# Performance work log

Measured on AMD Instinct MI355X. Metric: run time of the kernel, lower is better.

Reference implementation:

```python
import jax, jax.numpy as jnp
import numpy as np

NEG_SLOPE = 0.2  # PyG GATConv LeakyReLU slope
BN_EPS = 1e-5
NUM_GRAPHS = 16


def gat_conv(x, src, dst, W, a_src, a_dst, bias, heads, out_c, concat):
    N = x.shape[0]
    h = (x @ W).reshape(N, heads, out_c)                      # [N,H,C]
    s_src = jnp.sum(h * a_src, axis=-1)                       # [N,H] per-node src score
    s_dst = jnp.sum(h * a_dst, axis=-1)                       # [N,H]
    e = jax.nn.leaky_relu(s_src[src] + s_dst[dst], NEG_SLOPE) # [E,H]
    # segment softmax over incoming edges of each dst node
    m = jax.ops.segment_max(e, dst, num_segments=N)           # [N,H]
    ex = jnp.exp(e - m[dst])
    denom = jax.ops.segment_sum(ex, dst, num_segments=N)      # [N,H]
    alpha = ex / (denom[dst] + 1e-16)                         # [E,H]
    msg = h[src] * alpha[:, :, None]                          # [E,H,C]
    out = jax.ops.segment_sum(msg, dst, num_segments=N)       # [N,H,C]
    out = out.reshape(N, heads * out_c) if concat else out.mean(axis=1)
    return out + bias


def batchnorm_eval(x, gamma, beta, rm, rv):
    return (x - rm) * jax.lax.rsqrt(rv + BN_EPS) * gamma + beta


def setup_inputs() -> dict:
    key = jax.random.key(0)
    ks = jax.random.split(key, 16)
    N, E, Fin, Hc, Hd, Emb = 20000, 640000, 128, 64, 4, 128
    x = jax.random.normal(ks[0], (N, Fin), dtype=jnp.float32)
    edge_index = jax.random.randint(ks[1], (2, E), 0, N, dtype=jnp.int64)
    batch = jnp.sort(jax.random.randint(ks[2], (N,), 0, NUM_GRAPHS, dtype=jnp.int64))
    sc1 = 1.0 / np.sqrt(Fin)
    sc2 = 1.0 / np.sqrt(Hc * Hd)
    return {
        "x": x, "edge_index": edge_index, "batch": batch,
        "W1": jax.random.normal(ks[3], (Fin, Hd * Hc), dtype=jnp.float32) * sc1,
        "a_src1": jax.random.normal(ks[4], (Hd, Hc), dtype=jnp.float32) * sc2,
        "a_dst1": jax.random.normal(ks[5], (Hd, Hc), dtype=jnp.float32) * sc2,
        "b1": jnp.zeros((Hd * Hc,), jnp.float32),
        "g1": jnp.ones((Hd * Hc,), jnp.float32),
        "be1": jnp.zeros((Hd * Hc,), jnp.float32),
        "rm1": jax.random.normal(ks[6], (Hd * Hc,), dtype=jnp.float32) * 0.1,
        "rv1": jnp.ones((Hd * Hc,), jnp.float32),
        "W2": jax.random.normal(ks[7], (Hd * Hc, Emb), dtype=jnp.float32) * sc2,
        "a_src2": jax.random.normal(ks[8], (1, Emb), dtype=jnp.float32) / np.sqrt(Emb),
        "a_dst2": jax.random.normal(ks[9], (1, Emb), dtype=jnp.float32) / np.sqrt(Emb),
        "b2": jnp.zeros((Emb,), jnp.float32),
        "g2": jnp.ones((Emb,), jnp.float32),
        "be2": jnp.zeros((Emb,), jnp.float32),
        "rm2": jax.random.normal(ks[10], (Emb,), dtype=jnp.float32) * 0.1,
        "rv2": jnp.ones((Emb,), jnp.float32),
    }


def reference(x, edge_index, batch, W1, a_src1, a_dst1, b1, g1, be1, rm1, rv1,
              W2, a_src2, a_dst2, b2, g2, be2, rm2, rv2):
    N = x.shape[0]
    loops = jnp.arange(N, dtype=edge_index.dtype)
    src = jnp.concatenate([edge_index[0], loops])  # PyG GATConv adds self-loops
    dst = jnp.concatenate([edge_index[1], loops])
    # layer 1: heads=4, concat
    h = gat_conv(x, src, dst, W1, a_src1, a_dst1, b1, heads=4, out_c=64, concat=True)
    h = batchnorm_eval(h, g1, be1, rm1, rv1)
    h = jax.nn.elu(h)  # dropout is identity in eval mode
    # layer 2: heads=1, no concat (mean over heads)
    h = gat_conv(h, src, dst, W2, a_src2, a_dst2, b2, heads=1, out_c=128, concat=False)
    h = batchnorm_eval(h, g2, be2, rm2, rv2)
    # global mean pool per graph
    sums = jax.ops.segment_sum(h, batch, num_segments=NUM_GRAPHS)
    cnts = jax.ops.segment_sum(jnp.ones((N,), h.dtype), batch, num_segments=NUM_GRAPHS)
    return sums / jnp.maximum(cnts, 1.0)[:, None]
```

## Files before the change

kernel.cpp:

```cpp
#include <hip/hip_runtime.h>
#include <hip/hip_bf16.h>
#include <math.h>

#define NEG_SLOPE 0.2f
#define BN_EPS 1e-5f
#define ELLW 128
#define SCLAMP 60.0f
#define LDP 68

typedef __attribute__((ext_vector_type(8))) short bf16x8;
typedef __attribute__((ext_vector_type(4))) float f32x4;

__device__ __forceinline__ void atomAddF(float* p, float v) { unsafeAtomicAdd(p, v); }
__device__ __forceinline__ float bf_lo(unsigned u) { return __uint_as_float(u << 16); }
__device__ __forceinline__ float bf_hi(unsigned u) { return __uint_as_float(u & 0xffff0000u); }
__device__ __forceinline__ float lk(float x) { return x > 0.f ? x : NEG_SLOPE * x; }
__device__ __forceinline__ float eexp(float x) { return __expf(fminf(x, SCLAMP)); }

__global__ __launch_bounds__(256) void prep_kernel(const float* __restrict__ x,
                                                   const float* __restrict__ W1,
                                                   const float* __restrict__ W2,
                                                   const int* __restrict__ src,
                                                   const int* __restrict__ dst,
                                                   __hip_bfloat16* __restrict__ xbf,
                                                   __hip_bfloat16* __restrict__ WT1,
                                                   __hip_bfloat16* __restrict__ WT2,
                                                   int* __restrict__ cnt,
                                                   int* __restrict__ ell,
                                                   int n4, int E, int Etot) {
    int i = blockIdx.x * blockDim.x + threadIdx.x;
    if (i < n4) {
        float4 v = ((const float4*)x)[i];
        ushort4 st;
        st.x = __bfloat16_as_ushort(__float2bfloat16(v.x));
        st.y = __bfloat16_as_ushort(__float2bfloat16(v.y));
        st.z = __bfloat16_as_ushort(__float2bfloat16(v.z));
        st.w = __bfloat16_as_ushort(__float2bfloat16(v.w));
        *(ushort4*)(xbf + (size_t)i * 4) = st;
        return;
    }
    int j = i - n4;
    if (j < 128 * 256) {
        int k = j >> 8, n = j & 255;
        WT1[(size_t)n * 128 + k] = __float2bfloat16(W1[j]);
        return;
    }
    j -= 128 * 256;
    if (j < 256 * 128) {
        int k = j >> 7, n = j & 127;
        WT2[(size_t)n * 256 + k] = __float2bfloat16(W2[j]);
        return;
    }
    j -= 256 * 128;
    if (j < Etot) {
        int s, d;
        if (j < E) { s = src[j]; d = dst[j]; } else { s = d = j - E; }
        int pos = atomicAdd(cnt + d, 1);
        if (pos < ELLW) ell[(size_t)d * ELLW + pos] = s;
    }
}

__global__ __launch_bounds__(256) void gemm_score_kernel(const __hip_bfloat16* __restrict__ A,
                                                         const __hip_bfloat16* __restrict__ BT,
                                                         __hip_bfloat16* __restrict__ C,
                                                         const float* __restrict__ asrc,
                                                         const float* __restrict__ adst,
                                                         float* __restrict__ ssrc,
                                                         float* __restrict__ sdst,
                                                         int M, int N, int K, int heads) {
    __shared__ __hip_bfloat16 As[64 * LDP];
    __shared__ __hip_bfloat16 Bs[64 * LDP];
    const int tid = threadIdx.x;
    const int w = tid >> 6;
    const int lane = tid & 63;
    const int q = lane >> 4;
    const int r16 = lane & 15;
    const int bm = blockIdx.y * 64;
    const int bn = blockIdx.x * 64;
    const int lrow = tid >> 3;
    const int lseg = tid & 7;
    f32x4 acc[4] = {};

    for (int k0 = 0; k0 < K; k0 += 64) {
#pragma unroll
        for (int half = 0; half < 2; ++half) {
            int row = lrow + half * 32;
            int ga = min(bm + row, M - 1);
            *(bf16x8*)(&As[row * LDP + lseg * 8]) =
                *(const bf16x8*)(A + (size_t)ga * K + k0 + lseg * 8);
            *(bf16x8*)(&Bs[row * LDP + lseg * 8]) =
                *(const bf16x8*)(BT + (size_t)(bn + row) * K + k0 + lseg * 8);
        }
        __syncthreads();
#pragma unroll
        for (int kk = 0; kk < 64; kk += 32) {
            bf16x8 a = *(const bf16x8*)(&As[(w * 16 + r16) * LDP + kk + q * 8]);
#pragma unroll
            for (int t = 0; t < 4; ++t) {
                bf16x8 b = *(const bf16x8*)(&Bs[(t * 16 + r16) * LDP + kk + q * 8]);
                acc[t] = __builtin_amdgcn_mfma_f32_16x16x32_bf16(a, b, acc[t], 0, 0, 0);
            }
        }
        __syncthreads();
    }
#pragma unroll
    for (int t = 0; t < 4; ++t)
#pragma unroll
        for (int r = 0; r < 4; ++r) {
            int row = bm + w * 16 + q * 4 + r;
            if (row < M)
                C[(size_t)row * N + bn + t * 16 + r16] = __float2bfloat16(acc[t][r]);
        }
    if (heads) {
        const int h = (heads == 4) ? blockIdx.x : 0;
        float asv[4], adv[4];
#pragma unroll
        for (int t = 0; t < 4; ++t) {
            int col = bn + t * 16 + r16;
            asv[t] = asrc[col]; adv[t] = adst[col];
        }
#pragma unroll
        for (int r = 0; r < 4; ++r) {
            int row = bm + w * 16 + q * 4 + r;
            float ss = 0.f, sd = 0.f;
#pragma unroll
            for (int t = 0; t < 4; ++t) { ss += acc[t][r] * asv[t]; sd += acc[t][r] * adv[t]; }
#pragma unroll
            for (int mask = 1; mask <= 8; mask <<= 1) {
                ss += __shfl_xor(ss, mask);
                sd += __shfl_xor(sd, mask);
            }
            if (r16 == 0 && row < M) {
                atomAddF(&ssrc[(size_t)row * heads + h], ss);
                atomAddF(&sdst[(size_t)row * heads + h], sd);
            }
        }
    }
}

__global__ __launch_bounds__(256) void fused1_kernel(const int* __restrict__ ell,
                                                     const int* __restrict__ cnt,
                                                     const float* __restrict__ ssrc,
                                                     const float* __restrict__ sdst,
                                                     const __hip_bfloat16* __restrict__ h1,
                                                     const float* __restrict__ b,
                                                     const float* __restrict__ g,
                                                     const float* __restrict__ be,
                                                     const float* __restrict__ rm,
                                                     const float* __restrict__ rv,
                                                     __hip_bfloat16* __restrict__ out1,
                                                     int N) {
    __shared__ float4 sex[4][ELLW];
    const int w = threadIdx.x >> 6;
    const int lane = threadIdx.x & 63;
    const int n = blockIdx.x * 4 + w;
    if (n >= N) return;
    const int degn = min(cnt[n], ELLW);
    const int* __restrict__ row = ell + (size_t)n * ELLW;
    const float4 sd4 = *(const float4*)(sdst + (size_t)n * 4);

    float4 d4 = {0.f, 0.f, 0.f, 0.f};
    for (int i = lane; i < degn; i += 64) {
        int s = row[i];
        float4 sc = *(const float4*)(ssrc + (size_t)s * 4);
        float4 e4;
        e4.x = eexp(lk(sc.x + sd4.x)); e4.y = eexp(lk(sc.y + sd4.y));
        e4.z = eexp(lk(sc.z + sd4.z)); e4.w = eexp(lk(sc.w + sd4.w));
        sex[w][i] = e4;
        d4.x += e4.x; d4.y += e4.y; d4.z += e4.z; d4.w += e4.w;
    }
#pragma unroll
    for (int o = 32; o; o >>= 1) {
        d4.x += __shfl_xor(d4.x, o); d4.y += __shfl_xor(d4.y, o);
        d4.z += __shfl_xor(d4.z, o); d4.w += __shfl_xor(d4.w, o);
    }

    const int h = lane >> 4, c16 = lane & 15;
    const int ch = h * 64 + c16 * 4;
    const float denh = h == 0 ? d4.x : h == 1 ? d4.y : h == 2 ? d4.z : d4.w;
    const float rden = 1.f / (denh + 1e-16f);
    const __hip_bfloat16* hbase = h1 + ch;
    const float* exw = (const float*)&sex[w][0];

    f32x4 acc = {0.f, 0.f, 0.f, 0.f};
    int i = 0;
    for (; i + 7 < degn; i += 8) {
        int s[8]; float a[8]; uint2 u[8];
#pragma unroll
        for (int k = 0; k < 8; ++k) { s[k] = row[i + k]; a[k] = exw[(i + k) * 4 + h]; }
#pragma unroll
        for (int k = 0; k < 8; ++k) u[k] = *(const uint2*)(hbase + (size_t)s[k] * 256);
#pragma unroll
        for (int k = 0; k < 8; ++k) {
            acc.x += a[k] * bf_lo(u[k].x); acc.y += a[k] * bf_hi(u[k].x);
            acc.z += a[k] * bf_lo(u[k].y); acc.w += a[k] * bf_hi(u[k].y);
        }
    }
    for (; i < degn; ++i) {
        int s0 = row[i];
        float a0 = exw[i * 4 + h];
        uint2 u0 = *(const uint2*)(hbase + (size_t)s0 * 256);
        acc.x += a0 * bf_lo(u0.x); acc.y += a0 * bf_hi(u0.x);
        acc.z += a0 * bf_lo(u0.y); acc.w += a0 * bf_hi(u0.y);
    }
    float4 bb = *(const float4*)(b + ch), gg = *(const float4*)(g + ch);
    float4 ee = *(const float4*)(be + ch), mm = *(const float4*)(rm + ch);
    float4 vv = *(const float4*)(rv + ch);
    float o0 = (acc.x * rden + bb.x - mm.x) * rsqrtf(vv.x + BN_EPS) * gg.x + ee.x;
    float o1 = (acc.y * rden + bb.y - mm.y) * rsqrtf(vv.y + BN_EPS) * gg.y + ee.y;
    float o2 = (acc.z * rden + bb.z - mm.z) * rsqrtf(vv.z + BN_EPS) * gg.z + ee.z;
    float o3 = (acc.w * rden + bb.w - mm.w) * rsqrtf(vv.w + BN_EPS) * gg.w + ee.w;
    o0 = o0 > 0.f ? o0 : expm1f(o0);
    o1 = o1 > 0.f ? o1 : expm1f(o1);
    o2 = o2 > 0.f ? o2 : expm1f(o2);
    o3 = o3 > 0.f ? o3 : expm1f(o3);
    ushort4 st;
    st.x = __bfloat16_as_ushort(__float2bfloat16(o0));
    st.y = __bfloat16_as_ushort(__float2bfloat16(o1));
    st.z = __bfloat16_as_ushort(__float2bfloat16(o2));
    st.w = __bfloat16_as_ushort(__float2bfloat16(o3));
    *(ushort4*)(out1 + (size_t)n * 256 + ch) = st;
}

__global__ __launch_bounds__(256) void fused2_kernel(const int* __restrict__ ell,
                                                     const int* __restrict__ cnt,
                                                     const float* __restrict__ ssrc,
                                                     const float* __restrict__ sdst,
                                                     const __hip_bfloat16* __restrict__ h2,
                                                     const float* __restrict__ b,
                                                     const float* __restrict__ g,
                                                     const float* __restrict__ be,
                                                     const float* __restrict__ rm,
                                                     const float* __restrict__ rv,
                                                     float* __restrict__ out2,
                                                     int N) {
    __shared__ float sex[4][ELLW];
    const int w = threadIdx.x >> 6;
    const int lane = threadIdx.x & 63;
    const int n = blockIdx.x * 4 + w;
    if (n >= N) return;
    const int degn = min(cnt[n], ELLW);
    const int* __restrict__ row = ell + (size_t)n * ELLW;
    const float sd = sdst[n];

    float den = 0.f;
    for (int i = lane; i < degn; i += 64) {
        int s = row[i];
        float e = eexp(lk(ssrc[s] + sd));
        sex[w][i] = e;
        den += e;
    }
#pragma unroll
    for (int o = 32; o; o >>= 1) den += __shfl_xor(den, o);
    const float rden = 1.f / (den + 1e-16f);

    const int ch = lane * 2;
    const __hip_bfloat16* hbase = h2 + ch;
    float ax = 0.f, ay = 0.f;
    int i = 0;
    for (; i + 7 < degn; i += 8) {
        int s[8]; float a[8]; unsigned u[8];
#pragma unroll
        for (int k = 0; k < 8; ++k) { s[k] = row[i + k]; a[k] = sex[w][i + k]; }
#pragma unroll
        for (int k = 0; k < 8; ++k) u[k] = *(const unsigned*)(hbase + (size_t)s[k] * 128);
#pragma unroll
        for (int k = 0; k < 8; ++k) { ax += a[k] * bf_lo(u[k]); ay += a[k] * bf_hi(u[k]); }
    }
    for (; i < degn; ++i) {
        int s0 = row[i];
        float a0 = sex[w][i];
        unsigned u0 = *(const unsigned*)(hbase + (size_t)s0 * 128);
        ax += a0 * bf_lo(u0); ay += a0 * bf_hi(u0);
    }
    float2 bb = *(const float2*)(b + ch), gg = *(const float2*)(g + ch);
    float2 ee = *(const float2*)(be + ch), mm = *(const float2*)(rm + ch);
    float2 vv = *(const float2*)(rv + ch);
    float2 o;
    o.x = (ax * rden + bb.x - mm.x) * rsqrtf(vv.x + BN_EPS) * gg.x + ee.x;
    o.y = (ay * rden + bb.y - mm.y) * rsqrtf(vv.y + BN_EPS) * gg.y + ee.y;
    *(float2*)(out2 + (size_t)n * 128 + ch) = o;
}

__global__ __launch_bounds__(128) void pool_kernel(const float* __restrict__ out2,
                                                   const int* __restrict__ batch,
                                                   float* __restrict__ pool,
                                                   int N, int npb) {
    const int j = threadIdx.x;
    int n0 = blockIdx.x * npb;
    int n1 = min(n0 + npb, N);
    if (n0 >= n1) return;
    int curg = batch[n0];
    float acc = 0.f;
    for (int n = n0; n < n1; ++n) {
        int gr = batch[n];
        if (gr != curg) {
            atomAddF(pool + (size_t)curg * 128 + j, acc);
            acc = 0.f; curg = gr;
        }
        acc += out2[(size_t)n * 128 + j];
    }
    atomAddF(pool + (size_t)curg * 128 + j, acc);
}

__device__ __forceinline__ int lowerBound(const int* __restrict__ a, int n, int v) {
    int lo = 0, hi = n;
    while (lo < hi) {
        int mid = (lo + hi) >> 1;
        if (a[mid] < v) lo = mid + 1; else hi = mid;
    }
    return lo;
}

__global__ __launch_bounds__(256) void final_kernel(const float* __restrict__ pool,
                                                    const int* __restrict__ batch,
                                                    float* __restrict__ out, int N) {
    int i = blockIdx.x * blockDim.x + threadIdx.x;
    int g = i >> 7;
    int c = lowerBound(batch, N, g + 1) - lowerBound(batch, N, g);
    out[i] = pool[i] / fmaxf((float)c, 1.f);
}

extern "C" void kernel_launch(void* const* d_in, const int* in_sizes, int n_in,
                              void* d_out, int out_size, void* d_ws, size_t ws_size,
                              hipStream_t stream) {
    const float* x    = (const float*)d_in[0];
    const int* ei     = (const int*)d_in[1];
    const int* batch  = (const int*)d_in[2];
    const float* W1   = (const float*)d_in[3];
    const float* as1  = (const float*)d_in[4];
    const float* ad1  = (const float*)d_in[5];
    const float* b1   = (const float*)d_in[6];
    const float* g1   = (const float*)d_in[7];
    const float* be1  = (const float*)d_in[8];
    const float* rm1  = (const float*)d_in[9];
    const float* rv1  = (const float*)d_in[10];
    const float* W2   = (const float*)d_in[11];
    const float* as2  = (const float*)d_in[12];
    const float* ad2  = (const float*)d_in[13];
    const float* b2   = (const float*)d_in[14];
    const float* g2   = (const float*)d_in[15];
    const float* be2  = (const float*)d_in[16];
    const float* rm2  = (const float*)d_in[17];
    const float* rv2  = (const float*)d_in[18];
    float* out = (float*)d_out;

    const int N = in_sizes[0] / 128;
    const int E = in_sizes[1] / 2;
    const int Etot = E + N;
    const int* src = ei;
    const int* dst = ei + E;

    char* p = (char*)d_ws;
    auto alloc = [&](size_t bytes) { char* r = p; p += (bytes + 255) & ~(size_t)255; return r; };
    __hip_bfloat16* h1   = (__hip_bfloat16*)alloc((size_t)N * 256 * 2);
    __hip_bfloat16* out1 = (__hip_bfloat16*)alloc((size_t)N * 256 * 2);
    float* out2          = (float*)alloc((size_t)N * 128 * 4);
    __hip_bfloat16* xbf  = (__hip_bfloat16*)alloc((size_t)N * 128 * 2);
    __hip_bfloat16* WT1  = (__hip_bfloat16*)alloc(256 * 128 * 2);
    __hip_bfloat16* WT2  = (__hip_bfloat16*)alloc(128 * 256 * 2);
    char* zbase          = alloc((size_t)N * 10 * 4 + 2048 * 4 + (size_t)N * 4);
    float* ssrc1         = (float*)zbase;
    float* sdst1         = ssrc1 + (size_t)N * 4;
    float* ssrc2         = sdst1 + (size_t)N * 4;
    float* sdst2         = ssrc2 + N;
    float* pool          = sdst2 + N;
    int*   cnt           = (int*)(pool + 2048);
    int*   ell           = (int*)alloc((size_t)N * ELLW * 4);
    __hip_bfloat16* h2   = h1;

    const size_t zbytes = (size_t)N * 10 * 4 + 2048 * 4 + (size_t)N * 4;
    hipMemsetAsync(zbase, 0, zbytes, stream);

    const int n4 = N * 128 / 4;
    const int ptot = n4 + 2 * 128 * 256 + Etot;
    prep_kernel<<<(ptot + 255) / 256, 256, 0, stream>>>(x, W1, W2, src, dst, xbf, WT1, WT2,
                                                        cnt, ell, n4, E, Etot);

    gemm_score_kernel<<<dim3(256 / 64, (N + 63) / 64), 256, 0, stream>>>(
        xbf, WT1, h1, as1, ad1, ssrc1, sdst1, N, 256, 128, 4);
    fused1_kernel<<<(N + 3) / 4, 256, 0, stream>>>(ell, cnt, ssrc1, sdst1, h1,
                                                   b1, g1, be1, rm1, rv1, out1, N);
    gemm_score_kernel<<<dim3(128 / 64, (N + 63) / 64), 256, 0, stream>>>(
        out1, WT2, h2, as2, ad2, ssrc2, sdst2, N, 128, 256, 1);
    fused2_kernel<<<(N + 3) / 4, 256, 0, stream>>>(ell, cnt, ssrc2, sdst2, h2,
                                                   b2, g2, be2, rm2, rv2, out2, N);

    pool_kernel<<<(N + 19) / 20, 128, 0, stream>>>(out2, batch, pool, N, 20);
    final_kernel<<<8, 256, 0, stream>>>(pool, batch, out, N);
}
```

Measured before the change: 254.3 us.

## Split edge scatter into XCD-partitioned kernel with 16-bit ELL indices

Moves the edge-to-ELL scatter out of prep into its own kernel. Each block only handles destinations in the node range tied to its blockIdx modulo 8, so atomics and writes for a destination stay on one XCD's L2. ELL entries shrink from int to unsigned short, halving ELL writes and the reads in both fused kernels. Every block now reads the whole edge list, which is eight times the index traffic, and 16-bit indices only work while N fits under 65536.

```diff
diff --git a/kernel.cpp b/kernel.cpp
--- a/kernel.cpp
+++ b/kernel.cpp
@@ -20,14 +20,10 @@
 __global__ __launch_bounds__(256) void prep_kernel(const float* __restrict__ x,
                                                    const float* __restrict__ W1,
                                                    const float* __restrict__ W2,
-                                                   const int* __restrict__ src,
-                                                   const int* __restrict__ dst,
                                                    __hip_bfloat16* __restrict__ xbf,
                                                    __hip_bfloat16* __restrict__ WT1,
                                                    __hip_bfloat16* __restrict__ WT2,
-                                                   int* __restrict__ cnt,
-                                                   int* __restrict__ ell,
-                                                   int n4, int E, int Etot) {
+                                                   int n4) {
     int i = blockIdx.x * blockDim.x + threadIdx.x;
     if (i < n4) {
         float4 v = ((const float4*)x)[i];
@@ -49,14 +45,25 @@
     if (j < 256 * 128) {
         int k = j >> 7, n = j & 127;
         WT2[(size_t)n * 256 + k] = __float2bfloat16(W2[j]);
-        return;
-    }
-    j -= 256 * 128;
-    if (j < Etot) {
-        int s, d;
-        if (j < E) { s = src[j]; d = dst[j]; } else { s = d = j - E; }
+    }
+}
+
+__global__ __launch_bounds__(256) void scatter_kernel(const int* __restrict__ src,
+                                                      const int* __restrict__ dst,
+                                                      int* __restrict__ cnt,
+                                                      unsigned short* __restrict__ ell,
+                                                      int N, int E, int Etot) {
+    const int xcd = blockIdx.x & 7;
+    const int slice = blockIdx.x >> 3;
+    const int nslices = gridDim.x >> 3;
+    const int d0 = (int)((long)xcd * N / 8);
+    const int d1 = (int)((long)(xcd + 1) * N / 8);
+    for (int e = slice * 256 + threadIdx.x; e < Etot; e += nslices * 256) {
+        int d = (e < E) ? dst[e] : e - E;
+        if (d < d0 || d >= d1) continue;
+        int s = (e < E) ? src[e] : d;
         int pos = atomicAdd(cnt + d, 1);
-        if (pos < ELLW) ell[(size_t)d * ELLW + pos] = s;
+        if (pos < ELLW) ell[(size_t)d * ELLW + pos] = (unsigned short)s;
     }
 }
 
@@ -138,7 +145,7 @@
     }
 }
 
-__global__ __launch_bounds__(256) void fused1_kernel(const int* __restrict__ ell,
+__global__ __launch_bounds__(256) void fused1_kernel(const unsigned short* __restrict__ ell,
                                                      const int* __restrict__ cnt,
                                                      const float* __restrict__ ssrc,
                                                      const float* __restrict__ sdst,
@@ -156,7 +163,7 @@
     const int n = blockIdx.x * 4 + w;
     if (n >= N) return;
     const int degn = min(cnt[n], ELLW);
-    const int* __restrict__ row = ell + (size_t)n * ELLW;
+    const unsigned short* __restrict__ row = ell + (size_t)n * ELLW;
     const float4 sd4 = *(const float4*)(sdst + (size_t)n * 4);
 
     float4 d4 = {0.f, 0.f, 0.f, 0.f};
@@ -222,7 +229,7 @@
     *(ushort4*)(out1 + (size_t)n * 256 + ch) = st;
 }
 
-__global__ __launch_bounds__(256) void fused2_kernel(const int* __restrict__ ell,
+__global__ __launch_bounds__(256) void fused2_kernel(const unsigned short* __restrict__ ell,
                                                      const int* __restrict__ cnt,
                                                      const float* __restrict__ ssrc,
                                                      const float* __restrict__ sdst,
@@ -240,7 +247,7 @@
     const int n = blockIdx.x * 4 + w;
     if (n >= N) return;
     const int degn = min(cnt[n], ELLW);
-    const int* __restrict__ row = ell + (size_t)n * ELLW;
+    const unsigned short* __restrict__ row = ell + (size_t)n * ELLW;
     const float sd = sdst[n];
 
     float den = 0.f;
@@ -366,16 +373,16 @@
     float* sdst2         = ssrc2 + N;
     float* pool          = sdst2 + N;
     int*   cnt           = (int*)(pool + 2048);
-    int*   ell           = (int*)alloc((size_t)N * ELLW * 4);
+    unsigned short* ell  = (unsigned short*)alloc((size_t)N * ELLW * 2);
     __hip_bfloat16* h2   = h1;
 
     const size_t zbytes = (size_t)N * 10 * 4 + 2048 * 4 + (size_t)N * 4;
     hipMemsetAsync(zbase, 0, zbytes, stream);
 
     const int n4 = N * 128 / 4;
-    const int ptot = n4 + 2 * 128 * 256 + Etot;
-    prep_kernel<<<(ptot + 255) / 256, 256, 0, stream>>>(x, W1, W2, src, dst, xbf, WT1, WT2,
-                                                        cnt, ell, n4, E, Etot);
+    const int ptot = n4 + 2 * 128 * 256;
+    prep_kernel<<<(ptot + 255) / 256, 256, 0, stream>>>(x, W1, W2, xbf, WT1, WT2, n4);
+    scatter_kernel<<<2048, 256, 0, stream>>>(src, dst, cnt, ell, N, E, Etot);
 
     gemm_score_kernel<<<dim3(256 / 64, (N + 63) / 64), 256, 0, stream>>>(
         xbf, WT1, h1, as1, ad1, ssrc1, sdst1, N, 256, 128, 4);
```

New measurement: 244.1 us. -4.0%, faster.
